# Kernel optimization log

Measured on AMD Instinct MI355X. Metric: run time of the kernel, lower is better.

Reference implementation:

```python
import jax, jax.numpy as jnp
import numpy as np

BATCH = 256
INPUT_DIM = 512
OUTPUT_DIM = 512
NUM_WORKERS = 512
TOP_K = 154


def setup_inputs() -> dict:
    key = jax.random.key(0)
    k_x, k_gw, k_t = jax.random.split(key, 3)
    x = jax.random.normal(k_x, (BATCH, INPUT_DIM), dtype=jnp.float32)
    # router gate: nn.Linear(input_dim, num_workers), weight ~ N(0, 0.01), bias = 0
    gate_w = jax.random.normal(k_gw, (NUM_WORKERS, INPUT_DIM), dtype=jnp.float32) * 0.01
    gate_b = jnp.zeros((NUM_WORKERS,), dtype=jnp.float32)
    # 512 worker tiles, each [output_dim, input_dim], init randn*0.01
    tiles = jax.random.normal(k_t, (NUM_WORKERS, OUTPUT_DIM, INPUT_DIM), dtype=jnp.float32) * 0.01
    return {"x": x, "gate_w": gate_w, "gate_b": gate_b, "tiles": tiles}


def reference(x, gate_w, gate_b, tiles):
    B = x.shape[0]
    # Router: logits -> top-k -> softmax over selected scores
    gate_logits = x @ gate_w.T + gate_b                      # [B, E]
    scores, indices = jax.lax.top_k(gate_logits, TOP_K)      # [B, K]
    weights = jax.nn.softmax(scores, axis=-1)                # [B, K]
    # Scatter top-k weights into a dense [B, E] combine matrix (rest zero).
    w_full = jnp.zeros((B, NUM_WORKERS), dtype=x.dtype)
    w_full = w_full.at[jnp.arange(B)[:, None], indices].add(weights)
    # weight * (x @ tile.T) == (weight * x) @ tile.T  (linearity), so scale
    # inputs per (token, expert) and contract against all expert tiles.
    xw = w_full[:, :, None] * x[:, None, :]                  # [B, E, D]
    output = jnp.einsum('bed,eod->bo', xw, tiles)            # [B, O]
    return output
```

## Files before the change

### kernel.cpp

```cpp
#include <hip/hip_runtime.h>
#include <hip/hip_bf16.h>

#define B_ 256
#define D_ 512
#define E_ 512
#define K_ 154

typedef __attribute__((ext_vector_type(8))) short short8;
typedef __attribute__((ext_vector_type(4))) float f32x4;

__device__ __forceinline__ unsigned short f2bf(float f) {
    unsigned u = __float_as_uint(f);
    u = (u + 0x7fffu + ((u >> 16) & 1u)) >> 16;
    return (unsigned short)u;
}

__device__ __forceinline__ f32x4 ldnt4(const float* p) {
    return __builtin_nontemporal_load((const f32x4*)p);
}

__global__ __launch_bounds__(512) void k_gate(const float* __restrict__ x,
                                              const float* __restrict__ gw,
                                              double* __restrict__ logits) {
    const int tg = blockIdx.x;
    const int eg = blockIdx.y;
    const int tid = threadIdx.x;
    const int t0 = tg * 8, e0 = eg * 64;
    __shared__ double xs[8][512];
    __shared__ float gws[64][65];
    #pragma unroll
    for (int i = 0; i < 8; ++i) {
        int j = i * 512 + tid;
        xs[j >> 9][j & 511] = (double)x[(t0 + (j >> 9)) * D_ + (j & 511)];
    }
    const int e = tid & 63, tl = tid >> 6;
    double acc = 0.0;
    for (int dc = 0; dc < 8; ++dc) {
        __syncthreads();
        #pragma unroll
        for (int i = 0; i < 8; ++i) {
            int j = i * 512 + tid;
            gws[j >> 6][j & 63] = gw[(e0 + (j >> 6)) * D_ + dc * 64 + (j & 63)];
        }
        __syncthreads();
        #pragma unroll 8
        for (int d = 0; d < 64; ++d)
            acc = fma((double)gws[e][d], xs[tl][dc * 64 + d], acc);
    }
    logits[(t0 + tl) * E_ + e0 + e] = acc;
}

__global__ __launch_bounds__(512) void k_topk(const double* __restrict__ logits,
                                              const float* __restrict__ gb,
                                              const float* __restrict__ x,
                                              float* __restrict__ wT,
                                              unsigned short* __restrict__ xb) {
    const int b = blockIdx.x;
    const int e = threadIdx.x;
    __shared__ double vals[E_];
    __shared__ double red[512];
    double v = logits[b * E_ + e] + (double)gb[e];
    vals[e] = v;
    xb[b * D_ + e] = f2bf(x[b * D_ + e]);
    __syncthreads();
    int cnt = 0;
    double m = -1.0e300;
    for (int j = 0; j < E_; ++j) {
        double vj = vals[j];
        m = fmax(m, vj);
        cnt += (vj > v || (vj == v && j < e)) ? 1 : 0;
    }
    double p = (cnt < K_) ? exp(v - m) : 0.0;
    red[e] = p;
    __syncthreads();
    for (int s = 256; s > 0; s >>= 1) {
        if (e < s) red[e] += red[e + s];
        __syncthreads();
    }
    wT[e * B_ + b] = (float)(p / red[0]);
}

template <int EPG, bool TWO>
__global__ __launch_bounds__(256, 3) void k_moe(const unsigned short* __restrict__ xb,
                                                const float* __restrict__ wT,
                                                const float* __restrict__ tiles,
                                                float* __restrict__ dst) {
    const int nt = blockIdx.x & 15;
    const int g  = blockIdx.x >> 4;
    const int n0 = nt * 32;
    const int e0 = g * EPG;
    const int tid  = threadIdx.x;
    const int wv   = tid >> 6;
    const int lane = tid & 63;
    const int m0   = wv * 64;
    const int quad = lane >> 4;
    const int l16  = lane & 15;

    __shared__ __align__(16) unsigned short Bs[4 * 32 * 72];
    __shared__ float ws[EPG][B_];

    #pragma unroll
    for (int i = 0; i < EPG; ++i) {
        int idx = i * 256 + tid;
        ws[idx >> 8][idx & 255] = wT[(e0 + (idx >> 8)) * B_ + (idx & 255)];
    }

    f32x4 Ct[4][2];
    #pragma unroll
    for (int mi = 0; mi < 4; ++mi)
        #pragma unroll
        for (int ni = 0; ni < 2; ++ni)
            Ct[mi][ni] = (f32x4){0.f, 0.f, 0.f, 0.f};

    for (int kc = 0; kc < 8; ++kc) {
        const int k0 = kc * 64;
        short8 A[4][2];
        #pragma unroll
        for (int mi = 0; mi < 4; ++mi)
            #pragma unroll
            for (int ks = 0; ks < 2; ++ks)
                A[mi][ks] = *(const short8*)&xb[(m0 + mi * 16 + l16) * D_ + k0 + ks * 32 + quad * 8];

        for (int p = 0; p < EPG / 4; ++p) {
            const int ep = e0 + p * 4;
            __syncthreads();
            #pragma unroll
            for (int i = 0; i < 8; ++i) {
                int fi = (i * 256 + tid) * 4;
                int k  = fi & 63;
                int n  = (fi >> 6) & 31;
                int el = fi >> 11;
                const f32x4 f = ldnt4(tiles + ((ep + el) * D_ + (n0 + n)) * D_ + k0 + k);
                *(ushort4*)&Bs[(el * 32 + n) * 72 + k] =
                    make_ushort4(f2bf(f.x), f2bf(f.y), f2bf(f.z), f2bf(f.w));
            }
            __syncthreads();

            #pragma unroll
            for (int el = 0; el < 4; ++el) {
                f32x4 Ce[4][2];
                #pragma unroll
                for (int mi = 0; mi < 4; ++mi)
                    #pragma unroll
                    for (int ni = 0; ni < 2; ++ni)
                        Ce[mi][ni] = (f32x4){0.f, 0.f, 0.f, 0.f};
                #pragma unroll
                for (int ks = 0; ks < 2; ++ks) {
                    short8 Bf[2];
                    #pragma unroll
                    for (int ni = 0; ni < 2; ++ni)
                        Bf[ni] = *(const short8*)&Bs[(el * 32 + ni * 16 + l16) * 72 + ks * 32 + quad * 8];
                    #pragma unroll
                    for (int mi = 0; mi < 4; ++mi)
                        #pragma unroll
                        for (int ni = 0; ni < 2; ++ni)
                            Ce[mi][ni] = __builtin_amdgcn_mfma_f32_16x16x32_bf16(
                                A[mi][ks], Bf[ni], Ce[mi][ni], 0, 0, 0);
                }
                const float* wrow = ws[p * 4 + el];
                #pragma unroll
                for (int mi = 0; mi < 4; ++mi) {
                    const int rbase = m0 + mi * 16 + quad * 4;
                    float w0 = wrow[rbase + 0], w1 = wrow[rbase + 1];
                    float w2 = wrow[rbase + 2], w3 = wrow[rbase + 3];
                    #pragma unroll
                    for (int ni = 0; ni < 2; ++ni) {
                        Ct[mi][ni].x += w0 * Ce[mi][ni].x;
                        Ct[mi][ni].y += w1 * Ce[mi][ni].y;
                        Ct[mi][ni].z += w2 * Ce[mi][ni].z;
                        Ct[mi][ni].w += w3 * Ce[mi][ni].w;
                    }
                }
            }
        }
    }
    #pragma unroll
    for (int mi = 0; mi < 4; ++mi)
        #pragma unroll
        for (int ni = 0; ni < 2; ++ni) {
            const int row = m0 + mi * 16 + quad * 4;
            const int col = n0 + ni * 16 + l16;
            if (TWO) {
                float* base = dst + ((size_t)g * B_ + row) * D_ + col;
                __builtin_nontemporal_store(Ct[mi][ni].x, base + 0 * D_);
                __builtin_nontemporal_store(Ct[mi][ni].y, base + 1 * D_);
                __builtin_nontemporal_store(Ct[mi][ni].z, base + 2 * D_);
                __builtin_nontemporal_store(Ct[mi][ni].w, base + 3 * D_);
            } else {
                unsafeAtomicAdd(&dst[(row + 0) * D_ + col], Ct[mi][ni].x);
                unsafeAtomicAdd(&dst[(row + 1) * D_ + col], Ct[mi][ni].y);
                unsafeAtomicAdd(&dst[(row + 2) * D_ + col], Ct[mi][ni].z);
                unsafeAtomicAdd(&dst[(row + 3) * D_ + col], Ct[mi][ni].w);
            }
        }
}

template <int NG>
__global__ __launch_bounds__(256) void k_reduce(const float* __restrict__ P,
                                                float* __restrict__ out) {
    const int t = blockIdx.x * 256 + threadIdx.x;
    const f32x4* p4 = (const f32x4*)P;
    f32x4 acc = (f32x4){0.f, 0.f, 0.f, 0.f};
    #pragma unroll 8
    for (int gidx = 0; gidx < NG; ++gidx) {
        f32x4 v = __builtin_nontemporal_load(p4 + (size_t)gidx * 32768 + t);
        acc.x += v.x; acc.y += v.y; acc.z += v.z; acc.w += v.w;
    }
    ((f32x4*)out)[t] = acc;
}

extern "C" void kernel_launch(void* const* d_in, const int* in_sizes, int n_in,
                              void* d_out, int out_size, void* d_ws, size_t ws_size,
                              hipStream_t stream) {
    const float* x     = (const float*)d_in[0];
    const float* gw    = (const float*)d_in[1];
    const float* gb    = (const float*)d_in[2];
    const float* tiles = (const float*)d_in[3];
    float* out = (float*)d_out;

    char* base = (char*)d_ws;
    unsigned short* xb  = (unsigned short*)base;
    float* wT           = (float*)(base + 262144);
    double* logits      = (double*)(base + 262144 + 524288);
    float* P            = (float*)(base + 262144 + 524288);
    const size_t fixed  = 262144 + 524288;
    const size_t slot   = (size_t)B_ * D_ * sizeof(float);
    const size_t need16 = fixed + 32 * slot;
    const size_t need32 = fixed + 16 * slot;

    k_gate<<<dim3(32, 8), 512, 0, stream>>>(x, gw, logits);
    k_topk<<<256, 512, 0, stream>>>(logits, gb, x, wT, xb);
    if (ws_size >= need16) {
        k_moe<16, true><<<512, 256, 0, stream>>>(xb, wT, tiles, P);
        k_reduce<32><<<128, 256, 0, stream>>>(P, out);
    } else if (ws_size >= need32) {
        k_moe<32, true><<<256, 256, 0, stream>>>(xb, wT, tiles, P);
        k_reduce<16><<<128, 256, 0, stream>>>(P, out);
    } else {
        hipMemsetAsync(out, 0, (size_t)out_size * sizeof(float), stream);
        k_moe<8, false><<<1024, 256, 0, stream>>>(xb, wT, tiles, out);
    }
}
```

Measured before the change: 914.8 us.

## Load expert tile fragments directly from global into MFMA registers, drop LDS staging

Each wave now reads its B fragments straight from global memory as fp32, converts them with the packed v_cvt_pk_bf16_f32 instruction, and feeds them to the MFMA. This replaces the cooperative LDS staging with its two barriers per expert group. Because all four waves read the same tile fragments, global and L2 traffic per block rises about fourfold, and nontemporal loads are no longer used. Occupancy is relaxed from 3 to 2 blocks per SM to give more registers for in-flight loads. A missing sync after loading the weight table is also added.

```diff
diff --git a/kernel.cpp b/kernel.cpp
--- a/kernel.cpp
+++ b/kernel.cpp
@@ -15,8 +15,19 @@
     return (unsigned short)u;
 }
 
-__device__ __forceinline__ f32x4 ldnt4(const float* p) {
-    return __builtin_nontemporal_load((const f32x4*)p);
+__device__ __forceinline__ unsigned cvt_pk_bf16(float a, float b) {
+    unsigned r;
+    asm("v_cvt_pk_bf16_f32 %0, %1, %2" : "=v"(r) : "v"(a), "v"(b));
+    return r;
+}
+
+__device__ __forceinline__ short8 pack_bf16x8(f32x4 a, f32x4 b) {
+    union { unsigned u[4]; short8 s; } r;
+    r.u[0] = cvt_pk_bf16(a.x, a.y);
+    r.u[1] = cvt_pk_bf16(a.z, a.w);
+    r.u[2] = cvt_pk_bf16(b.x, b.y);
+    r.u[3] = cvt_pk_bf16(b.z, b.w);
+    return r.s;
 }
 
 __global__ __launch_bounds__(512) void k_gate(const float* __restrict__ x,
@@ -81,7 +92,7 @@
 }
 
 template <int EPG, bool TWO>
-__global__ __launch_bounds__(256, 3) void k_moe(const unsigned short* __restrict__ xb,
+__global__ __launch_bounds__(256, 2) void k_moe(const unsigned short* __restrict__ xb,
                                                 const float* __restrict__ wT,
                                                 const float* __restrict__ tiles,
                                                 float* __restrict__ dst) {
@@ -96,14 +107,13 @@
     const int quad = lane >> 4;
     const int l16  = lane & 15;
 
-    __shared__ __align__(16) unsigned short Bs[4 * 32 * 72];
     __shared__ float ws[EPG][B_];
-
     #pragma unroll
     for (int i = 0; i < EPG; ++i) {
         int idx = i * 256 + tid;
         ws[idx >> 8][idx & 255] = wT[(e0 + (idx >> 8)) * B_ + (idx & 255)];
     }
+    __syncthreads();
 
     f32x4 Ct[4][2];
     #pragma unroll
@@ -111,6 +121,8 @@
         #pragma unroll
         for (int ni = 0; ni < 2; ++ni)
             Ct[mi][ni] = (f32x4){0.f, 0.f, 0.f, 0.f};
+
+    const float* bp0 = tiles + ((size_t)e0 * D_ + n0 + l16) * D_ + quad * 8;
 
     for (int kc = 0; kc < 8; ++kc) {
         const int k0 = kc * 64;
@@ -121,55 +133,45 @@
             for (int ks = 0; ks < 2; ++ks)
                 A[mi][ks] = *(const short8*)&xb[(m0 + mi * 16 + l16) * D_ + k0 + ks * 32 + quad * 8];
 
-        for (int p = 0; p < EPG / 4; ++p) {
-            const int ep = e0 + p * 4;
-            __syncthreads();
-            #pragma unroll
-            for (int i = 0; i < 8; ++i) {
-                int fi = (i * 256 + tid) * 4;
-                int k  = fi & 63;
-                int n  = (fi >> 6) & 31;
-                int el = fi >> 11;
-                const f32x4 f = ldnt4(tiles + ((ep + el) * D_ + (n0 + n)) * D_ + k0 + k);
-                *(ushort4*)&Bs[(el * 32 + n) * 72 + k] =
-                    make_ushort4(f2bf(f.x), f2bf(f.y), f2bf(f.z), f2bf(f.w));
-            }
-            __syncthreads();
-
-            #pragma unroll
-            for (int el = 0; el < 4; ++el) {
-                f32x4 Ce[4][2];
+        const float* pk = bp0 + k0;
+        #pragma unroll 2
+        for (int e = 0; e < EPG; ++e) {
+            const float* pe = pk + (size_t)e * (D_ * D_);
+            f32x4 Ce[4][2];
+            #pragma unroll
+            for (int mi = 0; mi < 4; ++mi)
+                #pragma unroll
+                for (int ni = 0; ni < 2; ++ni)
+                    Ce[mi][ni] = (f32x4){0.f, 0.f, 0.f, 0.f};
+            #pragma unroll
+            for (int ks = 0; ks < 2; ++ks) {
+                short8 Bf[2];
+                #pragma unroll
+                for (int ni = 0; ni < 2; ++ni) {
+                    const float* q = pe + ni * (16 * D_) + ks * 32;
+                    f32x4 u = *(const f32x4*)q;
+                    f32x4 v = *(const f32x4*)(q + 4);
+                    Bf[ni] = pack_bf16x8(u, v);
+                }
                 #pragma unroll
                 for (int mi = 0; mi < 4; ++mi)
                     #pragma unroll
                     for (int ni = 0; ni < 2; ++ni)
-                        Ce[mi][ni] = (f32x4){0.f, 0.f, 0.f, 0.f};
-                #pragma unroll
-                for (int ks = 0; ks < 2; ++ks) {
-                    short8 Bf[2];
-                    #pragma unroll
-                    for (int ni = 0; ni < 2; ++ni)
-                        Bf[ni] = *(const short8*)&Bs[(el * 32 + ni * 16 + l16) * 72 + ks * 32 + quad * 8];
-                    #pragma unroll
-                    for (int mi = 0; mi < 4; ++mi)
-                        #pragma unroll
-                        for (int ni = 0; ni < 2; ++ni)
-                            Ce[mi][ni] = __builtin_amdgcn_mfma_f32_16x16x32_bf16(
-                                A[mi][ks], Bf[ni], Ce[mi][ni], 0, 0, 0);
-                }
-                const float* wrow = ws[p * 4 + el];
-                #pragma unroll
-                for (int mi = 0; mi < 4; ++mi) {
-                    const int rbase = m0 + mi * 16 + quad * 4;
-                    float w0 = wrow[rbase + 0], w1 = wrow[rbase + 1];
-                    float w2 = wrow[rbase + 2], w3 = wrow[rbase + 3];
-                    #pragma unroll
-                    for (int ni = 0; ni < 2; ++ni) {
-                        Ct[mi][ni].x += w0 * Ce[mi][ni].x;
-                        Ct[mi][ni].y += w1 * Ce[mi][ni].y;
-                        Ct[mi][ni].z += w2 * Ce[mi][ni].z;
-                        Ct[mi][ni].w += w3 * Ce[mi][ni].w;
-                    }
+                        Ce[mi][ni] = __builtin_amdgcn_mfma_f32_16x16x32_bf16(
+                            A[mi][ks], Bf[ni], Ce[mi][ni], 0, 0, 0);
+            }
+            const float* wrow = ws[e];
+            #pragma unroll
+            for (int mi = 0; mi < 4; ++mi) {
+                const int rbase = m0 + mi * 16 + quad * 4;
+                float w0 = wrow[rbase + 0], w1 = wrow[rbase + 1];
+                float w2 = wrow[rbase + 2], w3 = wrow[rbase + 3];
+                #pragma unroll
+                for (int ni = 0; ni < 2; ++ni) {
+                    Ct[mi][ni].x += w0 * Ce[mi][ni].x;
+                    Ct[mi][ni].y += w1 * Ce[mi][ni].y;
+                    Ct[mi][ni].z += w2 * Ce[mi][ni].z;
+                    Ct[mi][ni].w += w3 * Ce[mi][ni].w;
                 }
             }
         }
```

Result: faster. 896.5 us (-2.0%).

## Double-buffer tile staging in LDS with register prefetch and packed bf16 convert

Applied to the files above, without the earlier changes.

The MoE kernel now keeps two LDS buffers for the expert tiles. While the MFMAs run on the current buffer, it loads the next tile slice into registers and writes it into the other buffer, so there is one barrier per step instead of two. The fp32 to bf16 conversion now uses the hardware v_cvt_pk_bf16_f32 instruction instead of manual rounding, and the global load mapping is reorganised. Nontemporal loads and stores are replaced with ordinary ones, and launch bounds drop to 2 blocks per CU to make room for the extra prefetch registers and doubled LDS, which may lower occupancy.

```diff
diff --git a/kernel.cpp b/kernel.cpp
--- a/kernel.cpp
+++ b/kernel.cpp
@@ -15,8 +15,10 @@
     return (unsigned short)u;
 }
 
-__device__ __forceinline__ f32x4 ldnt4(const float* p) {
-    return __builtin_nontemporal_load((const f32x4*)p);
+__device__ __forceinline__ unsigned cvt_pk_bf16(float a, float b) {
+    unsigned r;
+    asm("v_cvt_pk_bf16_f32 %0, %1, %2" : "=v"(r) : "v"(a), "v"(b));
+    return r;
 }
 
 __global__ __launch_bounds__(512) void k_gate(const float* __restrict__ x,
@@ -81,7 +83,7 @@
 }
 
 template <int EPG, bool TWO>
-__global__ __launch_bounds__(256, 3) void k_moe(const unsigned short* __restrict__ xb,
+__global__ __launch_bounds__(256, 2) void k_moe(const unsigned short* __restrict__ xb,
                                                 const float* __restrict__ wT,
                                                 const float* __restrict__ tiles,
                                                 float* __restrict__ dst) {
@@ -95,9 +97,14 @@
     const int m0   = wv * 64;
     const int quad = lane >> 4;
     const int l16  = lane & 15;
-
-    __shared__ __align__(16) unsigned short Bs[4 * 32 * 72];
+    constexpr int PSTEPS = EPG / 4;
+    constexpr int NSTEP  = 8 * PSTEPS;
+
+    __shared__ __align__(16) unsigned short Bs[2][4 * 32 * 72];
     __shared__ float ws[EPG][B_];
+
+    const int srow = tid >> 4;
+    const int scol = (tid & 15) * 4;
 
     #pragma unroll
     for (int i = 0; i < EPG; ++i) {
@@ -111,6 +118,24 @@
         #pragma unroll
         for (int ni = 0; ni < 2; ++ni)
             Ct[mi][ni] = (f32x4){0.f, 0.f, 0.f, 0.f};
+
+    f32x4 st[8];
+    {
+        const float* sp = tiles + ((size_t)e0 * D_ + n0 + srow) * D_ + scol;
+        #pragma unroll
+        for (int i = 0; i < 8; ++i)
+            st[i] = *(const f32x4*)(sp + (size_t)(i >> 1) * (D_ * D_) + (i & 1) * (16 * D_));
+        #pragma unroll
+        for (int i = 0; i < 8; ++i) {
+            const int dr = (i >> 1) * 32 + (i & 1) * 16 + srow;
+            uint2 v2;
+            v2.x = cvt_pk_bf16(st[i].x, st[i].y);
+            v2.y = cvt_pk_bf16(st[i].z, st[i].w);
+            *(uint2*)&Bs[0][dr * 72 + scol] = v2;
+        }
+    }
+    __syncthreads();
+    int cur = 0;
 
     for (int kc = 0; kc < 8; ++kc) {
         const int k0 = kc * 64;
@@ -121,21 +146,21 @@
             for (int ks = 0; ks < 2; ++ks)
                 A[mi][ks] = *(const short8*)&xb[(m0 + mi * 16 + l16) * D_ + k0 + ks * 32 + quad * 8];
 
-        for (int p = 0; p < EPG / 4; ++p) {
-            const int ep = e0 + p * 4;
-            __syncthreads();
-            #pragma unroll
-            for (int i = 0; i < 8; ++i) {
-                int fi = (i * 256 + tid) * 4;
-                int k  = fi & 63;
-                int n  = (fi >> 6) & 31;
-                int el = fi >> 11;
-                const f32x4 f = ldnt4(tiles + ((ep + el) * D_ + (n0 + n)) * D_ + k0 + k);
-                *(ushort4*)&Bs[(el * 32 + n) * 72 + k] =
-                    make_ushort4(f2bf(f.x), f2bf(f.y), f2bf(f.z), f2bf(f.w));
-            }
-            __syncthreads();
-
+        #pragma unroll 1
+        for (int p = 0; p < PSTEPS; ++p) {
+            const int s = kc * PSTEPS + p;
+            const bool pre = (s + 1 < NSTEP);
+            if (pre) {
+                const int np  = (p + 1 < PSTEPS) ? p + 1 : 0;
+                const int nkc = (p + 1 < PSTEPS) ? kc : kc + 1;
+                const float* sp = tiles + ((size_t)(e0 + np * 4) * D_ + n0 + srow) * D_
+                                + nkc * 64 + scol;
+                #pragma unroll
+                for (int i = 0; i < 8; ++i)
+                    st[i] = *(const f32x4*)(sp + (size_t)(i >> 1) * (D_ * D_) + (i & 1) * (16 * D_));
+            }
+
+            const unsigned short* bsrc = Bs[cur];
             #pragma unroll
             for (int el = 0; el < 4; ++el) {
                 f32x4 Ce[4][2];
@@ -149,7 +174,7 @@
                     short8 Bf[2];
                     #pragma unroll
                     for (int ni = 0; ni < 2; ++ni)
-                        Bf[ni] = *(const short8*)&Bs[(el * 32 + ni * 16 + l16) * 72 + ks * 32 + quad * 8];
+                        Bf[ni] = *(const short8*)&bsrc[(el * 32 + ni * 16 + l16) * 72 + ks * 32 + quad * 8];
                     #pragma unroll
                     for (int mi = 0; mi < 4; ++mi)
                         #pragma unroll
@@ -172,8 +197,23 @@
                     }
                 }
             }
-        }
-    }
+
+            if (pre) {
+                unsigned short* bdst = Bs[cur ^ 1];
+                #pragma unroll
+                for (int i = 0; i < 8; ++i) {
+                    const int dr = (i >> 1) * 32 + (i & 1) * 16 + srow;
+                    uint2 v2;
+                    v2.x = cvt_pk_bf16(st[i].x, st[i].y);
+                    v2.y = cvt_pk_bf16(st[i].z, st[i].w);
+                    *(uint2*)&bdst[dr * 72 + scol] = v2;
+                }
+            }
+            __syncthreads();
+            cur ^= 1;
+        }
+    }
+
     #pragma unroll
     for (int mi = 0; mi < 4; ++mi)
         #pragma unroll
@@ -182,10 +222,10 @@
             const int col = n0 + ni * 16 + l16;
             if (TWO) {
                 float* base = dst + ((size_t)g * B_ + row) * D_ + col;
-                __builtin_nontemporal_store(Ct[mi][ni].x, base + 0 * D_);
-                __builtin_nontemporal_store(Ct[mi][ni].y, base + 1 * D_);
-                __builtin_nontemporal_store(Ct[mi][ni].z, base + 2 * D_);
-                __builtin_nontemporal_store(Ct[mi][ni].w, base + 3 * D_);
+                base[0 * D_] = Ct[mi][ni].x;
+                base[1 * D_] = Ct[mi][ni].y;
+                base[2 * D_] = Ct[mi][ni].z;
+                base[3 * D_] = Ct[mi][ni].w;
             } else {
                 unsafeAtomicAdd(&dst[(row + 0) * D_ + col], Ct[mi][ni].x);
                 unsafeAtomicAdd(&dst[(row + 1) * D_ + col], Ct[mi][ni].y);
@@ -203,7 +243,7 @@
     f32x4 acc = (f32x4){0.f, 0.f, 0.f, 0.f};
     #pragma unroll 8
     for (int gidx = 0; gidx < NG; ++gidx) {
-        f32x4 v = __builtin_nontemporal_load(p4 + (size_t)gidx * 32768 + t);
+        f32x4 v = p4[(size_t)gidx * 32768 + t];
         acc.x += v.x; acc.y += v.y; acc.z += v.z; acc.w += v.w;
     }
     ((f32x4*)out)[t] = acc;
```

New measurement: 1.103 ms. 20.5% more time.
